# Kernel tuning notes

Measured on AMD Instinct MI355X. Metric: run time of the kernel, lower is better.

Reference implementation:

```python
import jax, jax.numpy as jnp
import numpy as np

B, K, N, F, H = 20000, 10, 100000, 256, 128


def setup_inputs() -> dict:
    key = jax.random.key(0)
    ks = jax.random.split(key, 8)
    neighbors = jax.random.randint(ks[0], (B, K), 0, N)
    embed_table = jax.random.normal(ks[1], (N, F), dtype=jnp.float32)
    w = lambda k, shp: jax.random.normal(k, shp, dtype=jnp.float32) * 0.05
    return {
        "neighbors": neighbors,
        "embed_table": embed_table,
        "W1a": w(ks[2], (F, H)), "W1b": w(ks[3], (H, H)),
        "W2a": w(ks[4], (F, H)), "W2b": w(ks[5], (H, H)),
        "W3a": w(ks[6], (F, H)), "W3b": w(ks[7], (H, H)),
    }


def reference(neighbors, embed_table, W1a, W1b, W2a, W2b, W3a, W3b):
    # Gather each batch node's K sampled neighbor embeddings: [B, K, F]
    x = embed_table[neighbors]
    # Three MLP projections: Linear(F,H,no bias) -> tanh -> Linear(H,H,no bias)
    q = jnp.tanh(x @ W1a) @ W1b              # [B, K, H]  (att1)
    k = jnp.tanh(x @ W2a) @ W2b              # [B, K, H]  (att2)
    v = jnp.tanh(x @ W3a) @ W3b              # [B, K, H]  (att3)
    # Per-node attention over the K neighbors, softmax along last dim
    att = jax.nn.softmax(jnp.einsum('bid,bjd->bij', q, k), axis=-1)  # [B, K, K]
    # torch: sum over rows of (att @ v) -> contract both i and j
    out = jnp.einsum('bij,bjd->bd', att, v)  # [B, H]
    return out
```

## Files before the change

### kernel.cpp

```cpp
#include <hip/hip_runtime.h>
#include <hip/hip_bf16.h>

constexpr int B_ = 20000;
constexpr int K_ = 10;
constexpr int N_ = 100000;
constexpr int F_ = 256;
constexpr int H_ = 128;
constexpr int RW = 3 * H_;

typedef __attribute__((ext_vector_type(8))) short bf16x8;
typedef __attribute__((ext_vector_type(4))) float f32x4;
typedef __attribute__((ext_vector_type(4))) unsigned short ushort4v;

__device__ __forceinline__ unsigned short f2bf(float x) {
  unsigned int u = __builtin_bit_cast(unsigned int, x);
  unsigned int r = u + 0x7fffu + ((u >> 16) & 1u);
  return (unsigned short)(r >> 16);
}

__device__ __forceinline__ float bf2f(unsigned int u16) {
  return __builtin_bit_cast(float, u16 << 16);
}

__device__ __forceinline__ unsigned int cvt_pk_bf16(float lo, float hi) {
  unsigned int r;
  asm("v_cvt_pk_bf16_f32 %0, %1, %2" : "=v"(r) : "v"(lo), "v"(hi));
  return r;
}

__device__ __forceinline__ float fast_tanh(float x) {
  float e = __expf(2.0f * x);
  return 1.0f - 2.0f * __builtin_amdgcn_rcpf(e + 1.0f);
}

__global__ __launch_bounds__(256) void prep_kernel(
    const float* __restrict__ W1a, const float* __restrict__ W1b,
    const float* __restrict__ W2a, const float* __restrict__ W2b,
    const float* __restrict__ W3a, const float* __restrict__ W3b,
    unsigned short* __restrict__ wat2, unsigned short* __restrict__ wbt2) {
  const float* Wa[3] = {W1a, W2a, W3a};
  const float* Wb[3] = {W1b, W2b, W3b};
  int g = blockIdx.x * 256 + threadIdx.x;
  if (g < 3 * 64 * 512) {
    int chunk = g >> 9;
    int e = g & 511;
    int lane = e >> 3, j = e & 7;
    int c = chunk & 7;
    int ks = (chunk >> 3) & 7;
    int p = chunk >> 6;
    int k = 32 * ks + 8 * (lane >> 4) + j;
    int h = 16 * c + (lane & 15);
    wat2[g] = f2bf(Wa[p][k * H_ + h]);
  } else {
    int g2 = g - 3 * 64 * 512;
    int chunk = g2 >> 9;
    int e = g2 & 511;
    int lane = e >> 3, j = e & 7;
    int ks2 = chunk & 3;
    int c2 = (chunk >> 2) & 7;
    int p = chunk >> 5;
    int k = 32 * ks2 + 8 * (lane >> 4) + j;
    int h2 = 16 * c2 + (lane & 15);
    wbt2[g2] = f2bf(Wb[p][k * H_ + h2]);
  }
}

constexpr int MT = 32;
constexpr int XS = F_ + 8;
constexpr int TS = H_ + 8;

__global__ __launch_bounds__(256) void proj_kernel(
    const float* __restrict__ E,
    const unsigned short* __restrict__ wat2,
    const unsigned short* __restrict__ wbt2,
    unsigned short* __restrict__ qkvI) {
  __shared__ unsigned short xs[MT * XS];
  __shared__ unsigned short ts[MT * TS];

  const int tid = threadIdx.x;
  const int lane = tid & 63;
  const int w = tid >> 6;
  const int l15 = lane & 15;
  const int q = lane >> 4;
  const int row0 = blockIdx.x * MT;

  {
    const float4* Eg = (const float4*)E;
#pragma unroll
    for (int it = 0; it < 8; ++it) {
      int i = tid + 256 * it;
      int r = i >> 6;
      int c4 = i & 63;
      int row = row0 + r;
      if (row >= N_) row = N_ - 1;
      float4 v = Eg[(size_t)row * (F_ / 4) + c4];
      unsigned int lo = cvt_pk_bf16(v.x, v.y);
      unsigned int hi = cvt_pk_bf16(v.z, v.w);
      *(uint2*)&xs[r * XS + c4 * 4] = make_uint2(lo, hi);
    }
  }
  __syncthreads();

  for (int p = 0; p < 3; ++p) {
    const unsigned short* __restrict__ wa = wat2 + p * (64 * 512);
    const unsigned short* __restrict__ wb = wbt2 + p * (32 * 512);

    f32x4 acc[2][2];
#pragma unroll
    for (int i = 0; i < 2; ++i)
#pragma unroll
      for (int j = 0; j < 2; ++j) acc[i][j] = (f32x4)0.0f;

#pragma unroll
    for (int ks = 0; ks < 8; ++ks) {
      bf16x8 af0 = *(const bf16x8*)&wa[(ks * 8 + 2 * w) * 512 + lane * 8];
      bf16x8 af1 = *(const bf16x8*)&wa[(ks * 8 + 2 * w + 1) * 512 + lane * 8];
      bf16x8 bx0 = *(const bf16x8*)&xs[(l15)*XS + 32 * ks + 8 * q];
      bf16x8 bx1 = *(const bf16x8*)&xs[(16 + l15) * XS + 32 * ks + 8 * q];
      acc[0][0] = __builtin_amdgcn_mfma_f32_16x16x32_bf16(af0, bx0, acc[0][0], 0, 0, 0);
      acc[0][1] = __builtin_amdgcn_mfma_f32_16x16x32_bf16(af0, bx1, acc[0][1], 0, 0, 0);
      acc[1][0] = __builtin_amdgcn_mfma_f32_16x16x32_bf16(af1, bx0, acc[1][0], 0, 0, 0);
      acc[1][1] = __builtin_amdgcn_mfma_f32_16x16x32_bf16(af1, bx1, acc[1][1], 0, 0, 0);
    }

    __syncthreads();
#pragma unroll
    for (int i = 0; i < 2; ++i)
#pragma unroll
      for (int j = 0; j < 2; ++j) {
        unsigned int lo = cvt_pk_bf16(fast_tanh(acc[i][j][0]), fast_tanh(acc[i][j][1]));
        unsigned int hi = cvt_pk_bf16(fast_tanh(acc[i][j][2]), fast_tanh(acc[i][j][3]));
        *(uint2*)&ts[(16 * j + l15) * TS + 16 * (2 * w + i) + 4 * q] =
            make_uint2(lo, hi);
      }
    __syncthreads();

    f32x4 ac2[2][2];
#pragma unroll
    for (int i = 0; i < 2; ++i)
#pragma unroll
      for (int j = 0; j < 2; ++j) ac2[i][j] = (f32x4)0.0f;

#pragma unroll
    for (int ks2 = 0; ks2 < 4; ++ks2) {
      bf16x8 ab0 = *(const bf16x8*)&wb[((2 * w) * 4 + ks2) * 512 + lane * 8];
      bf16x8 ab1 = *(const bf16x8*)&wb[((2 * w + 1) * 4 + ks2) * 512 + lane * 8];
      bf16x8 bt0 = *(const bf16x8*)&ts[(l15)*TS + 32 * ks2 + 8 * q];
      bf16x8 bt1 = *(const bf16x8*)&ts[(16 + l15) * TS + 32 * ks2 + 8 * q];
      ac2[0][0] = __builtin_amdgcn_mfma_f32_16x16x32_bf16(ab0, bt0, ac2[0][0], 0, 0, 0);
      ac2[0][1] = __builtin_amdgcn_mfma_f32_16x16x32_bf16(ab0, bt1, ac2[0][1], 0, 0, 0);
      ac2[1][0] = __builtin_amdgcn_mfma_f32_16x16x32_bf16(ab1, bt0, ac2[1][0], 0, 0, 0);
      ac2[1][1] = __builtin_amdgcn_mfma_f32_16x16x32_bf16(ab1, bt1, ac2[1][1], 0, 0, 0);
    }

#pragma unroll
    for (int i = 0; i < 2; ++i)
#pragma unroll
      for (int j = 0; j < 2; ++j) {
        int n = row0 + 16 * j + l15;
        if (n < N_) {
          unsigned int lo = cvt_pk_bf16(ac2[i][j][0], ac2[i][j][1]);
          unsigned int hi = cvt_pk_bf16(ac2[i][j][2], ac2[i][j][3]);
          *(uint2*)&qkvI[(size_t)n * RW + p * H_ + 16 * (2 * w + i) + 4 * q] =
              make_uint2(lo, hi);
        }
      }
  }
}

__global__ __launch_bounds__(256) void agg_kernel(
    const int* __restrict__ nbr,
    const unsigned short* __restrict__ qkvI,
    float* __restrict__ out) {
  const int lane = threadIdx.x & 63;
  const int wv = threadIdx.x >> 6;
  const int b = blockIdx.x * 4 + wv;
  const int l15 = lane & 15;
  const int kg = lane >> 4;

  const int ni = nbr[b * K_ + (l15 < K_ ? l15 : 0)];
  const size_t nbase = (size_t)ni * RW;

  f32x4 sc = (f32x4)0.0f;
#pragma unroll
  for (int k = 0; k < 4; ++k) {
    const int off = k * 32 + kg * 8;
    bf16x8 qf = *(const bf16x8*)&qkvI[nbase + off];
    bf16x8 kf = *(const bf16x8*)&qkvI[nbase + H_ + off];
    sc = __builtin_amdgcn_mfma_f32_16x16x32_bf16(qf, kf, sc, 0, 0, 0);
  }

  if (l15 >= K_) {
#pragma unroll
    for (int r = 0; r < 4; ++r) sc[r] = -3.0e38f;
  }

  float mx[4], e[4], sm[4];
#pragma unroll
  for (int r = 0; r < 4; ++r) mx[r] = sc[r];
#pragma unroll
  for (int st = 1; st < 16; st <<= 1)
#pragma unroll
    for (int r = 0; r < 4; ++r) mx[r] = fmaxf(mx[r], __shfl_xor(mx[r], st, 16));
#pragma unroll
  for (int r = 0; r < 4; ++r) { e[r] = __expf(sc[r] - mx[r]); sm[r] = e[r]; }
#pragma unroll
  for (int st = 1; st < 16; st <<= 1)
#pragma unroll
    for (int r = 0; r < 4; ++r) sm[r] += __shfl_xor(sm[r], st, 16);

  float cs = 0.0f;
#pragma unroll
  for (int r = 0; r < 4; ++r) {
    float a = e[r] * __builtin_amdgcn_rcpf(sm[r]);
    if (kg * 4 + r >= K_) a = 0.0f;
    cs += a;
  }
  cs += __shfl_xor(cs, 16, 64);
  cs += __shfl_xor(cs, 32, 64);

  float o0 = 0.0f, o1 = 0.0f;
#pragma unroll
  for (int j = 0; j < K_; ++j) {
    const float cj = __shfl(cs, j, 64);
    const int nj = __shfl(ni, j, 64);
    const unsigned int v2 =
        *(const unsigned int*)&qkvI[(size_t)nj * RW + 2 * H_ + 2 * lane];
    o0 = fmaf(cj, bf2f(v2 & 0xffffu), o0);
    o1 = fmaf(cj, bf2f(v2 >> 16), o1);
  }
  *(float2*)&out[(size_t)b * H_ + 2 * lane] = make_float2(o0, o1);
}

extern "C" void kernel_launch(void* const* d_in, const int* in_sizes, int n_in,
                              void* d_out, int out_size, void* d_ws, size_t ws_size,
                              hipStream_t stream) {
  const int* nbr = (const int*)d_in[0];
  const float* E = (const float*)d_in[1];
  const float* W1a = (const float*)d_in[2];
  const float* W1b = (const float*)d_in[3];
  const float* W2a = (const float*)d_in[4];
  const float* W2b = (const float*)d_in[5];
  const float* W3a = (const float*)d_in[6];
  const float* W3b = (const float*)d_in[7];
  float* out = (float*)d_out;

  unsigned short* qkvI = (unsigned short*)d_ws;
  unsigned short* wat2 = qkvI + (size_t)N_ * RW;
  unsigned short* wbt2 = wat2 + (size_t)3 * 64 * 512;

  prep_kernel<<<(3 * 64 * 512 + 3 * 32 * 512) / 256, 256, 0, stream>>>(
      W1a, W1b, W2a, W2b, W3a, W3b, wat2, wbt2);
  proj_kernel<<<N_ / MT, 256, 0, stream>>>(E, wat2, wbt2, qkvI);
  agg_kernel<<<B_ / 4, 256, 0, stream>>>(nbr, qkvI, out);
}
```

Baseline: 237.2 us.

## Enlarge projection tile to 64 rows with 16 waves per block

```diff
diff --git a/kernel.cpp b/kernel.cpp
--- a/kernel.cpp
+++ b/kernel.cpp
@@ -65,11 +65,11 @@
   }
 }
 
-constexpr int MT = 32;
+constexpr int MT = 64;
 constexpr int XS = F_ + 8;
 constexpr int TS = H_ + 8;
 
-__global__ __launch_bounds__(256) void proj_kernel(
+__global__ __launch_bounds__(1024) void proj_kernel(
     const float* __restrict__ E,
     const unsigned short* __restrict__ wat2,
     const unsigned short* __restrict__ wbt2,
@@ -80,6 +80,8 @@
   const int tid = threadIdx.x;
   const int lane = tid & 63;
   const int w = tid >> 6;
+  const int g = w >> 3;
+  const int hp = w & 7;
   const int l15 = lane & 15;
   const int q = lane >> 4;
   const int row0 = blockIdx.x * MT;
@@ -87,8 +89,8 @@
   {
     const float4* Eg = (const float4*)E;
 #pragma unroll
-    for (int it = 0; it < 8; ++it) {
-      int i = tid + 256 * it;
+    for (int it = 0; it < 4; ++it) {
+      int i = tid + 1024 * it;
       int r = i >> 6;
       int c4 = i & 63;
       int row = row0 + r;
@@ -105,66 +107,52 @@
     const unsigned short* __restrict__ wa = wat2 + p * (64 * 512);
     const unsigned short* __restrict__ wb = wbt2 + p * (32 * 512);
 
-    f32x4 acc[2][2];
-#pragma unroll
-    for (int i = 0; i < 2; ++i)
-#pragma unroll
-      for (int j = 0; j < 2; ++j) acc[i][j] = (f32x4)0.0f;
+    f32x4 acc[2];
+    acc[0] = (f32x4)0.0f;
+    acc[1] = (f32x4)0.0f;
 
 #pragma unroll
     for (int ks = 0; ks < 8; ++ks) {
-      bf16x8 af0 = *(const bf16x8*)&wa[(ks * 8 + 2 * w) * 512 + lane * 8];
-      bf16x8 af1 = *(const bf16x8*)&wa[(ks * 8 + 2 * w + 1) * 512 + lane * 8];
-      bf16x8 bx0 = *(const bf16x8*)&xs[(l15)*XS + 32 * ks + 8 * q];
-      bf16x8 bx1 = *(const bf16x8*)&xs[(16 + l15) * XS + 32 * ks + 8 * q];
-      acc[0][0] = __builtin_amdgcn_mfma_f32_16x16x32_bf16(af0, bx0, acc[0][0], 0, 0, 0);
-      acc[0][1] = __builtin_amdgcn_mfma_f32_16x16x32_bf16(af0, bx1, acc[0][1], 0, 0, 0);
-      acc[1][0] = __builtin_amdgcn_mfma_f32_16x16x32_bf16(af1, bx0, acc[1][0], 0, 0, 0);
-      acc[1][1] = __builtin_amdgcn_mfma_f32_16x16x32_bf16(af1, bx1, acc[1][1], 0, 0, 0);
+      bf16x8 af = *(const bf16x8*)&wa[(ks * 8 + hp) * 512 + lane * 8];
+      bf16x8 bx0 = *(const bf16x8*)&xs[(16 * (2 * g) + l15) * XS + 32 * ks + 8 * q];
+      bf16x8 bx1 = *(const bf16x8*)&xs[(16 * (2 * g + 1) + l15) * XS + 32 * ks + 8 * q];
+      acc[0] = __builtin_amdgcn_mfma_f32_16x16x32_bf16(af, bx0, acc[0], 0, 0, 0);
+      acc[1] = __builtin_amdgcn_mfma_f32_16x16x32_bf16(af, bx1, acc[1], 0, 0, 0);
     }
 
     __syncthreads();
 #pragma unroll
-    for (int i = 0; i < 2; ++i)
-#pragma unroll
-      for (int j = 0; j < 2; ++j) {
-        unsigned int lo = cvt_pk_bf16(fast_tanh(acc[i][j][0]), fast_tanh(acc[i][j][1]));
-        unsigned int hi = cvt_pk_bf16(fast_tanh(acc[i][j][2]), fast_tanh(acc[i][j][3]));
-        *(uint2*)&ts[(16 * j + l15) * TS + 16 * (2 * w + i) + 4 * q] =
+    for (int j = 0; j < 2; ++j) {
+      unsigned int lo = cvt_pk_bf16(fast_tanh(acc[j][0]), fast_tanh(acc[j][1]));
+      unsigned int hi = cvt_pk_bf16(fast_tanh(acc[j][2]), fast_tanh(acc[j][3]));
+      *(uint2*)&ts[(16 * (2 * g + j) + l15) * TS + 16 * hp + 4 * q] =
+          make_uint2(lo, hi);
+    }
+    __syncthreads();
+
+    f32x4 ac2[2];
+    ac2[0] = (f32x4)0.0f;
+    ac2[1] = (f32x4)0.0f;
+
+#pragma unroll
+    for (int ks2 = 0; ks2 < 4; ++ks2) {
+      bf16x8 ab = *(const bf16x8*)&wb[(hp * 4 + ks2) * 512 + lane * 8];
+      bf16x8 bt0 = *(const bf16x8*)&ts[(16 * (2 * g) + l15) * TS + 32 * ks2 + 8 * q];
+      bf16x8 bt1 = *(const bf16x8*)&ts[(16 * (2 * g + 1) + l15) * TS + 32 * ks2 + 8 * q];
+      ac2[0] = __builtin_amdgcn_mfma_f32_16x16x32_bf16(ab, bt0, ac2[0], 0, 0, 0);
+      ac2[1] = __builtin_amdgcn_mfma_f32_16x16x32_bf16(ab, bt1, ac2[1], 0, 0, 0);
+    }
+
+#pragma unroll
+    for (int j = 0; j < 2; ++j) {
+      int n = row0 + 16 * (2 * g + j) + l15;
+      if (n < N_) {
+        unsigned int lo = cvt_pk_bf16(ac2[j][0], ac2[j][1]);
+        unsigned int hi = cvt_pk_bf16(ac2[j][2], ac2[j][3]);
+        *(uint2*)&qkvI[(size_t)n * RW + p * H_ + 16 * hp + 4 * q] =
             make_uint2(lo, hi);
       }
-    __syncthreads();
-
-    f32x4 ac2[2][2];
-#pragma unroll
-    for (int i = 0; i < 2; ++i)
-#pragma unroll
-      for (int j = 0; j < 2; ++j) ac2[i][j] = (f32x4)0.0f;
-
-#pragma unroll
-    for (int ks2 = 0; ks2 < 4; ++ks2) {
-      bf16x8 ab0 = *(const bf16x8*)&wb[((2 * w) * 4 + ks2) * 512 + lane * 8];
-      bf16x8 ab1 = *(const bf16x8*)&wb[((2 * w + 1) * 4 + ks2) * 512 + lane * 8];
-      bf16x8 bt0 = *(const bf16x8*)&ts[(l15)*TS + 32 * ks2 + 8 * q];
-      bf16x8 bt1 = *(const bf16x8*)&ts[(16 + l15) * TS + 32 * ks2 + 8 * q];
-      ac2[0][0] = __builtin_amdgcn_mfma_f32_16x16x32_bf16(ab0, bt0, ac2[0][0], 0, 0, 0);
-      ac2[0][1] = __builtin_amdgcn_mfma_f32_16x16x32_bf16(ab0, bt1, ac2[0][1], 0, 0, 0);
-      ac2[1][0] = __builtin_amdgcn_mfma_f32_16x16x32_bf16(ab1, bt0, ac2[1][0], 0, 0, 0);
-      ac2[1][1] = __builtin_amdgcn_mfma_f32_16x16x32_bf16(ab1, bt1, ac2[1][1], 0, 0, 0);
-    }
-
-#pragma unroll
-    for (int i = 0; i < 2; ++i)
-#pragma unroll
-      for (int j = 0; j < 2; ++j) {
-        int n = row0 + 16 * j + l15;
-        if (n < N_) {
-          unsigned int lo = cvt_pk_bf16(ac2[i][j][0], ac2[i][j][1]);
-          unsigned int hi = cvt_pk_bf16(ac2[i][j][2], ac2[i][j][3]);
-          *(uint2*)&qkvI[(size_t)n * RW + p * H_ + 16 * (2 * w + i) + 4 * q] =
-              make_uint2(lo, hi);
-        }
-      }
+    }
   }
 }
 
@@ -251,6 +239,6 @@
 
   prep_kernel<<<(3 * 64 * 512 + 3 * 32 * 512) / 256, 256, 0, stream>>>(
       W1a, W1b, W2a, W2b, W3a, W3b, wat2, wbt2);
-  proj_kernel<<<N_ / MT, 256, 0, stream>>>(E, wat2, wbt2, qkvI);
+  proj_kernel<<<(N_ + MT - 1) / MT, 1024, 0, stream>>>(E, wat2, wbt2, qkvI);
   agg_kernel<<<B_ / 4, 256, 0, stream>>>(nbr, qkvI, out);
 }
```

After: 245.6 us. +3.6%, slower.
